# Kernel optimization log

Measured on AMD Instinct MI355X. Metric: run time of the kernel, lower is better.

Reference implementation:

```python
import jax, jax.numpy as jnp
import numpy as np

N = 50000      # nodes in batched graph
E = 800000     # edges
IN_DIM = 16
HID = 64
NH = 4         # heads
G = 128        # graphs in batch
OUT_DIM = 32
NUM_LAYERS = 8
NEG_SLOPE = 0.2  # DGL GATv2Conv default


def setup_inputs() -> dict:
    key = jax.random.key(0)
    ks = jax.random.split(key, 12)
    feat = jax.random.normal(ks[0], (N, IN_DIM), dtype=jnp.float32)
    src = jax.random.randint(ks[1], (E,), 0, N, dtype=jnp.int32)
    dst = jax.random.randint(ks[2], (E,), 0, N, dtype=jnp.int32)
    graph_ids = jnp.sort(jax.random.randint(ks[3], (N,), 0, G, dtype=jnp.int32))
    is_root = jax.random.randint(ks[4], (N,), 0, 2, dtype=jnp.int32)
    s_in = 1.0 / np.sqrt(IN_DIM)
    s_h = 1.0 / np.sqrt(2 * HID)
    s_o = 1.0 / np.sqrt(HID)
    return {
        'feat': feat, 'src': src, 'dst': dst,
        'graph_ids': graph_ids, 'is_root': is_root,
        'W_in': jax.random.normal(ks[5], (IN_DIM, HID), jnp.float32) * s_in,
        'b_in': jnp.zeros((HID,), jnp.float32),
        'W_src': jax.random.normal(ks[6], (2 * HID, NH * HID), jnp.float32) * s_h,
        'b_src': jnp.zeros((NH * HID,), jnp.float32),
        'W_dst': jax.random.normal(ks[7], (2 * HID, NH * HID), jnp.float32) * s_h,
        'b_dst': jnp.zeros((NH * HID,), jnp.float32),
        'attn': jax.random.normal(ks[8], (NH, HID), jnp.float32) * s_o,
        'W_out': jax.random.normal(ks[9], (HID, OUT_DIM), jnp.float32) * s_o,
        'b_out': jnp.zeros((OUT_DIM,), jnp.float32),
    }


def reference(feat, src, dst, graph_ids, is_root,
              W_in, b_in, W_src, b_src, W_dst, b_dst, attn, W_out, b_out):
    h0 = feat @ W_in + b_in                       # [N, HID]
    h = h0
    for _ in range(NUM_LAYERS):
        x = jnp.concatenate([h, h0], axis=1)      # [N, 2*HID]
        fs = (x @ W_src + b_src).reshape(-1, NH, HID)  # [N, NH, HID]
        fd = (x @ W_dst + b_dst).reshape(-1, NH, HID)
        # per-edge GATv2 attention logits
        e = jax.nn.leaky_relu(fs[src] + fd[dst], NEG_SLOPE)   # [E, NH, HID]
        s = jnp.einsum('ehd,hd->eh', e, attn)                 # [E, NH]
        # segment softmax over incoming edges of each dst node
        m = jax.ops.segment_max(s, dst, num_segments=N)       # [N, NH]
        a = jnp.exp(s - m[dst])
        denom = jax.ops.segment_sum(a, dst, num_segments=N)
        alpha = a / denom[dst]                                # [E, NH]
        # weighted aggregation of source features
        agg = jax.ops.segment_sum(alpha[:, :, None] * fs[src], dst,
                                  num_segments=N)             # [N, NH, HID]
        h = jnp.tanh(agg).sum(axis=1)                         # [N, HID]
    # root-weighted readout per graph
    hg = jax.ops.segment_sum(h * is_root.astype(h.dtype)[:, None],
                             graph_ids, num_segments=G)       # [G, HID]
    return hg @ W_out + b_out                                 # [G, OUT_DIM]
```

## Files before the change

kernel.cpp:

```cpp
#include <hip/hip_runtime.h>
#include <math.h>

#define N_NODES 50000
#define N_EDGES 800000
#define IN_DIM  16
#define HID     64
#define NH      4
#define NGRAPH  128
#define OUT_DIM 32
#define NUM_LAYERS 8
#define NEG_SLOPE 0.2f

#define SCAN_BLOCKS ((N_NODES + 255) / 256)

typedef unsigned short u16;
typedef _Float16 h2   __attribute__((ext_vector_type(2)));
typedef _Float16 f16x8 __attribute__((ext_vector_type(8)));
typedef __attribute__((ext_vector_type(4))) float f32x4;

static __device__ __forceinline__ u16 f2h(float f) {
    _Float16 h = (_Float16)f; u16 r; __builtin_memcpy(&r, &h, 2); return r;
}
static __device__ __forceinline__ float h2f_lo(unsigned w) {
    _Float16 h; u16 u = (u16)w; __builtin_memcpy(&h, &u, 2); return (float)h;
}
static __device__ __forceinline__ h2 shfl_h2(h2 v, int mask) {
    int i; __builtin_memcpy(&i, &v, 4); i = __shfl_xor(i, mask);
    h2 r; __builtin_memcpy(&r, &i, 4); return r;
}
static __device__ __forceinline__ h2 bcast_h2(float f) {
    _Float16 h = (_Float16)f; h2 r; r[0] = h; r[1] = h; return r;
}

#define DPP_XOR1(x) __uint_as_float((unsigned)__builtin_amdgcn_update_dpp(0, (int)__float_as_uint(x), 0xB1, 0xF, 0xF, true))
#define DPP_XOR2(x) __uint_as_float((unsigned)__builtin_amdgcn_update_dpp(0, (int)__float_as_uint(x), 0x4E, 0xF, 0xF, true))


__global__ void k_build_wpack(const float* __restrict__ Wsrc, const float* __restrict__ bsrc,
                              const float* __restrict__ Wdst, const float* __restrict__ bdst,
                              const float* __restrict__ attn,
                              u16* __restrict__ Wpack, float* __restrict__ bcat,
                              u16* __restrict__ an_h) {
    int tid = blockIdx.x * 256 + threadIdx.x;
    int i = tid & 7;
    int l = (tid >> 3) & 63;
    int rest = tid >> 9;
    int kt = rest & 3;
    int nt = rest >> 2;
    int k = kt * 32 + (l >> 4) * 8 + i;
    int col = nt * 16 + (l & 15);
    float v = (col < 256) ? Wsrc[k * 256 + col] : Wdst[k * 256 + (col - 256)];
    Wpack[tid] = f2h(v);
    if (tid < 512) bcat[tid] = (tid < 256) ? bsrc[tid] : bdst[tid - 256];
    if (tid < 256) an_h[tid] = f2h(attn[tid] * 1.44269504f);
}

__global__ void k_hist(const int* __restrict__ dst, int* __restrict__ deg) {
    int e = blockIdx.x * 256 + threadIdx.x;
    if (e < N_EDGES) atomicAdd(&deg[dst[e]], 1);
}

__global__ void k_blocksum(const int* __restrict__ deg, int* __restrict__ bsum) {
    __shared__ int sm[256];
    int i = blockIdx.x * 256 + threadIdx.x;
    sm[threadIdx.x] = (i < N_NODES) ? deg[i] : 0;
    __syncthreads();
    for (int s = 128; s > 0; s >>= 1) {
        if (threadIdx.x < s) sm[threadIdx.x] += sm[threadIdx.x + s];
        __syncthreads();
    }
    if (threadIdx.x == 0) bsum[blockIdx.x] = sm[0];
}

__global__ void k_scanbsum(int* __restrict__ bsum) {
    if (threadIdx.x == 0 && blockIdx.x == 0) {
        int acc = 0;
        for (int b = 0; b < SCAN_BLOCKS; b++) { int t = bsum[b]; bsum[b] = acc; acc += t; }
    }
}

__global__ void k_rowptr(const int* __restrict__ deg, const int* __restrict__ bsum,
                         int* __restrict__ row_ptr) {
    __shared__ int sm[256];
    int i = blockIdx.x * 256 + threadIdx.x;
    int v = (i < N_NODES) ? deg[i] : 0;
    sm[threadIdx.x] = v;
    __syncthreads();
    for (int s = 1; s < 256; s <<= 1) {
        int t = (threadIdx.x >= (unsigned)s) ? sm[threadIdx.x - s] : 0;
        __syncthreads();
        sm[threadIdx.x] += t;
        __syncthreads();
    }
    if (i < N_NODES) row_ptr[i] = bsum[blockIdx.x] + sm[threadIdx.x] - v;
}

__global__ void k_scatter(const int* __restrict__ src, const int* __restrict__ dst,
                          const int* __restrict__ row_ptr, int* __restrict__ cursor,
                          int* __restrict__ csr_src) {
    int e = blockIdx.x * 256 + threadIdx.x;
    if (e < N_EDGES) {
        int d = dst[e];
        int pos = atomicAdd(&cursor[d], 1);
        csr_src[row_ptr[d] + pos] = src[e];
    }
}

__global__ __launch_bounds__(256) void k_in_gemm(const float* __restrict__ feat,
                                                 const float* __restrict__ W,
                                                 const float* __restrict__ b,
                                                 u16* __restrict__ h0h) {
    __shared__ float sW[IN_DIM * HID];
    __shared__ float sb[HID];
    int t = threadIdx.x;
    for (int i = t; i < IN_DIM * HID; i += 256) sW[i] = W[i];
    if (t < HID) sb[t] = b[t];
    __syncthreads();
    int wid = (blockIdx.x * 256 + t) >> 6;
    int lane = t & 63;
    const float* f = feat + wid * IN_DIM;
    float acc = sb[lane];
    #pragma unroll
    for (int k = 0; k < IN_DIM; k++) acc += f[k] * sW[k * HID + lane];
    h0h[wid * HID + lane] = f2h(acc);
}


#define ST_STRIDE 152
__global__ __launch_bounds__(256) void k_gemm_mfma(const u16* __restrict__ hb,
                                                   const u16* __restrict__ h0b,
                                                   const u16* __restrict__ Wpack,
                                                   const float* __restrict__ bcat,
                                                   u16* __restrict__ fsfd) {
    __shared__ u16 smem[16384];
    int tid = threadIdx.x;
    int l = tid & 63, w = tid >> 6;
    int lr = l & 15, lg = l >> 4;
    int wave_gid = blockIdx.x * 4 + w;
    size_t rbase = (size_t)wave_gid * 32;
    u16* myst = smem + w * 4096;

    for (int g = 0; g < 4; g++) {
        __syncthreads();
        {
            const f16x8* src = (const f16x8*)(Wpack) + g * 2048;
            f16x8* dst = (f16x8*)smem;
            #pragma unroll
            for (int it = 0; it < 8; it++) dst[it * 256 + tid] = src[it * 256 + tid];
        }
        __syncthreads();

        f32x4 acc[2][8];
        #pragma unroll
        for (int rt = 0; rt < 2; rt++)
            #pragma unroll
            for (int nt = 0; nt < 8; nt++) acc[rt][nt] = (f32x4){0.f, 0.f, 0.f, 0.f};

        #pragma unroll
        for (int kt = 0; kt < 4; kt++) {
            const u16* A = (kt < 2) ? hb : h0b;
            int koff = (kt & 1) * 32 + lg * 8;
            f16x8 a0, a1;
            {
                size_t r0 = rbase + lr;
                size_t r1 = rbase + 16 + lr;
                if (r0 >= N_NODES) r0 = 0;
                if (r1 >= N_NODES) r1 = 0;
                a0 = *(const f16x8*)(A + r0 * HID + koff);
                a1 = *(const f16x8*)(A + r1 * HID + koff);
            }
            #pragma unroll
            for (int nt = 0; nt < 8; nt++) {
                f16x8 bfr = *(const f16x8*)(smem + nt * 2048 + kt * 512 + l * 8);
                acc[0][nt] = __builtin_amdgcn_mfma_f32_16x16x32_f16(a0, bfr, acc[0][nt], 0, 0, 0);
                acc[1][nt] = __builtin_amdgcn_mfma_f32_16x16x32_f16(a1, bfr, acc[1][nt], 0, 0, 0);
            }
        }
        __syncthreads();

        #pragma unroll
        for (int rt = 0; rt < 2; rt++) {
            size_t row0 = rbase + rt * 16;
            if (row0 >= N_NODES) break;
            #pragma unroll
            for (int nt = 0; nt < 8; nt++) {
                float bv = bcat[g * 128 + nt * 16 + lr];
                #pragma unroll
                for (int j = 0; j < 4; j++)
                    myst[(lg * 4 + j) * ST_STRIDE + nt * 16 + lr] = f2h(acc[rt][nt][j] + bv);
            }
            #pragma unroll
            for (int j = 0; j < 4; j++) {
                int rloc = j * 4 + lg;
                f16x8 v = *(const f16x8*)(myst + rloc * ST_STRIDE + lr * 8);
                *(f16x8*)(fsfd + (row0 + rloc) * 512 + g * 128 + lr * 8) = v;
            }
        }
    }
}

__global__ __launch_bounds__(256) void k_edge(const u16* __restrict__ fsfd,
                                              const u16* __restrict__ an_h,
                                              const int* __restrict__ row_ptr,
                                              const int* __restrict__ deg,
                                              const int* __restrict__ csr_src,
                                              u16* __restrict__ h) {
    int wid = (blockIdx.x * 256 + threadIdx.x) >> 6;
    int lane = threadIdx.x & 63;
    int g  = lane >> 4;
    int ll = lane & 15;
    const size_t ebase = (size_t)ll * 16;

    h2 an[8], fdh[8];
    {
        const uint4* ap = (const uint4*)(an_h + ebase);
        uint4 a0 = ap[0], a1 = ap[1];
        unsigned aw[8] = {a0.x, a0.y, a0.z, a0.w, a1.x, a1.y, a1.z, a1.w};
        __builtin_memcpy(an, aw, 32);
        const uint4* fp = (const uint4*)(fsfd + (size_t)wid * 512 + 256 + ebase);
        uint4 b0 = fp[0], b1 = fp[1];
        unsigned fw[8] = {b0.x, b0.y, b0.z, b0.w, b1.x, b1.y, b1.z, b1.w};
        __builtin_memcpy(fdh, fw, 32);
    }
    const h2 slope2 = {(_Float16)NEG_SLOPE, (_Float16)NEG_SLOPE};

    float m = -3.0e38f, denom = 0.f;
    h2 agg[8];
    #pragma unroll
    for (int q = 0; q < 8; q++) agg[q] = (h2){(_Float16)0.f, (_Float16)0.f};

    int r0 = row_ptr[wid], dg = deg[wid];
    for (int i = g; i < dg; i += 4) {
        int s = csr_src[r0 + i];
        const uint4* P = (const uint4*)(fsfd + (size_t)s * 512 + ebase);
        uint4 A = P[0], B = P[1];
        h2 f[8];
        {
            unsigned fw[8] = {A.x, A.y, A.z, A.w, B.x, B.y, B.z, B.w};
            __builtin_memcpy(f, fw, 32);
        }
        float p = 0.f;
        #pragma unroll
        for (int q = 0; q < 8; q++) {
            h2 e  = f[q] + fdh[q];
            h2 lk = __builtin_elementwise_max(e, e * slope2);
#if __has_builtin(__builtin_amdgcn_fdot2)
            p = __builtin_amdgcn_fdot2(lk, an[q], p, false);
#else
            h2 pr = lk * an[q];
            p += (float)pr[0] + (float)pr[1];
#endif
        }
        p += DPP_XOR1(p);
        p += DPP_XOR2(p);
        float nm = fmaxf(m, p);
        float rs = exp2f(m - nm);
        float c  = exp2f(p - nm);
        h2 rs2 = bcast_h2(rs), c2 = bcast_h2(c);
        #pragma unroll
        for (int q = 0; q < 8; q++) agg[q] = agg[q] * rs2 + f[q] * c2;
        denom = fmaf(denom, rs, c);
        m = nm;
    }

    #pragma unroll
    for (int mask = 16; mask <= 32; mask <<= 1) {
        float mo = __shfl_xor(m, mask);
        float dn = __shfl_xor(denom, mask);
        float nm = fmaxf(m, mo);
        float sa = exp2f(m - nm);
        float sb = exp2f(mo - nm);
        h2 sa2 = bcast_h2(sa), sb2 = bcast_h2(sb);
        denom = denom * sa + dn * sb;
        #pragma unroll
        for (int q = 0; q < 8; q++)
            agg[q] = agg[q] * sa2 + shfl_h2(agg[q], mask) * sb2;
        m = nm;
    }

    float inv = denom > 0.f ? __builtin_amdgcn_rcpf(denom) : 0.f;
    float t[16];
    #pragma unroll
    for (int q = 0; q < 8; q++) {
        #pragma unroll
        for (int j = 0; j < 2; j++) {
            float x = (float)agg[q][j] * inv;
            float E = exp2f(x * 2.885390082f);
            float r = __builtin_amdgcn_rcpf(E + 1.f);
            float v = fmaf(-2.f, r, 1.f);
            v += __shfl_xor(v, 4);
            v += __shfl_xor(v, 8);
            t[q * 2 + j] = v;
        }
    }
    if (lane < 4) {
        unsigned o[8];
        #pragma unroll
        for (int q = 0; q < 8; q++)
            o[q] = (unsigned)f2h(t[2*q]) | ((unsigned)f2h(t[2*q+1]) << 16);
        u16* hp = h + (size_t)wid * 64 + lane * 16;
        *(uint4*)hp       = make_uint4(o[0], o[1], o[2], o[3]);
        *(uint4*)(hp + 8) = make_uint4(o[4], o[5], o[6], o[7]);
    }
}


__global__ __launch_bounds__(256) void k_readout(const u16* __restrict__ h,
                                                 const int* __restrict__ graph_ids,
                                                 const int* __restrict__ is_root,
                                                 float* __restrict__ hg) {
    int wid = (blockIdx.x * 256 + threadIdx.x) >> 6;
    int lane = threadIdx.x & 63;
    if (is_root[wid]) {
        int g = graph_ids[wid];
        atomicAdd(&hg[g * HID + lane], h2f_lo(h[(size_t)wid * HID + lane]));
    }
}

__global__ void k_out_gemm(const float* __restrict__ hg, const float* __restrict__ W,
                           const float* __restrict__ b, float* __restrict__ out) {
    int i = blockIdx.x * 256 + threadIdx.x;
    if (i >= NGRAPH * OUT_DIM) return;
    int g = i >> 5, o = i & 31;
    float acc = b[o];
    #pragma unroll
    for (int k = 0; k < HID; k++) acc += hg[g * HID + k] * W[k * OUT_DIM + o];
    out[i] = acc;
}


extern "C" void kernel_launch(void* const* d_in, const int* in_sizes, int n_in,
                              void* d_out, int out_size, void* d_ws, size_t ws_size,
                              hipStream_t stream) {
    const float* feat      = (const float*)d_in[0];
    const int*   src       = (const int*)d_in[1];
    const int*   dst       = (const int*)d_in[2];
    const int*   graph_ids = (const int*)d_in[3];
    const int*   is_root   = (const int*)d_in[4];
    const float* W_in      = (const float*)d_in[5];
    const float* b_in      = (const float*)d_in[6];
    const float* W_src     = (const float*)d_in[7];
    const float* b_src     = (const float*)d_in[8];
    const float* W_dst     = (const float*)d_in[9];
    const float* b_dst     = (const float*)d_in[10];
    const float* attn      = (const float*)d_in[11];
    const float* W_out     = (const float*)d_in[12];
    const float* b_out     = (const float*)d_in[13];
    float* out = (float*)d_out;

    char* base = (char*)d_ws;
    size_t off = 0;
    auto carve = [&](size_t bytes) -> char* {
        char* p = base + off;
        off = (off + bytes + 255) & ~(size_t)255;
        return p;
    };
    u16*   h0b     = (u16*)carve((size_t)N_NODES * HID * 2);
    u16*   hb      = (u16*)carve((size_t)N_NODES * HID * 2);
    u16*   fsfd    = (u16*)carve((size_t)N_NODES * 512 * 2);
    u16*   Wpack   = (u16*)carve(128 * 512 * 2);
    float* bcat    = (float*)carve(512 * 4);
    u16*   an_h    = (u16*)carve(256 * 2);
    int*   csr_src = (int*)carve((size_t)N_EDGES * 4);
    int*   row_ptr = (int*)carve((size_t)N_NODES * 4);
    int*   bsum    = (int*)carve(SCAN_BLOCKS * 4);
    char*  zero0   = carve(0);
    int*   deg     = (int*)carve((size_t)N_NODES * 4);
    int*   cursor  = (int*)carve((size_t)N_NODES * 4);
    float* hg      = (float*)carve((size_t)NGRAPH * HID * 4);
    char*  zero1   = base + off;
    if (off > ws_size) return;

    hipMemsetAsync(zero0, 0, (size_t)(zero1 - zero0), stream);

    k_build_wpack<<<256, 256, 0, stream>>>(W_src, b_src, W_dst, b_dst, attn, Wpack, bcat, an_h);
    k_hist<<<(N_EDGES + 255) / 256, 256, 0, stream>>>(dst, deg);
    k_blocksum<<<SCAN_BLOCKS, 256, 0, stream>>>(deg, bsum);
    k_scanbsum<<<1, 64, 0, stream>>>(bsum);
    k_rowptr<<<SCAN_BLOCKS, 256, 0, stream>>>(deg, bsum, row_ptr);
    k_scatter<<<(N_EDGES + 255) / 256, 256, 0, stream>>>(src, dst, row_ptr, cursor, csr_src);

    k_in_gemm<<<N_NODES / 4, 256, 0, stream>>>(feat, W_in, b_in, h0b);

    const int gemm_grid = (N_NODES + 127) / 128;
    for (int layer = 0; layer < NUM_LAYERS; layer++) {
        const u16* hcur = (layer == 0) ? h0b : hb;
        k_gemm_mfma<<<gemm_grid, 256, 0, stream>>>(hcur, h0b, Wpack, bcat, fsfd);
        k_edge<<<N_NODES / 4, 256, 0, stream>>>(fsfd, an_h, row_ptr, deg, csr_src, hb);
    }

    k_readout<<<N_NODES / 4, 256, 0, stream>>>(hb, graph_ids, is_root, hg);
    k_out_gemm<<<(NGRAPH * OUT_DIM + 255) / 256, 256, 0, stream>>>(hg, W_out, b_out, out);
}
```

Measured before the change: 948.7 us.

## Unroll edge loop two-way with dual softmax accumulators and split tanh epilogue

The per-node attention/aggregation kernel now processes two edges per lane group per iteration, issuing both gathers up front and keeping two independent online-softmax states that are merged after the loop. This gives more memory-level parallelism and shorter dependency chains. The cross-group merge now does a max-rescale followed by plain sums, and the tanh epilogue is split so each lane group computes 4 of the 16 values instead of all 16, cutting redundant transcendental work and shuffles. The cost is higher register pressure and a duplicated, clamped load when the second edge is out of range.

```diff
diff --git a/kernel.cpp b/kernel.cpp
--- a/kernel.cpp
+++ b/kernel.cpp
@@ -224,83 +224,130 @@
     }
     const h2 slope2 = {(_Float16)NEG_SLOPE, (_Float16)NEG_SLOPE};
 
-    float m = -3.0e38f, denom = 0.f;
-    h2 agg[8];
+    float mA = -3.0e38f, mB = -3.0e38f, dnA = 0.f, dnB = 0.f;
+    h2 aggA[8], aggB[8];
     #pragma unroll
-    for (int q = 0; q < 8; q++) agg[q] = (h2){(_Float16)0.f, (_Float16)0.f};
+    for (int q = 0; q < 8; q++) {
+        aggA[q] = (h2){(_Float16)0.f, (_Float16)0.f};
+        aggB[q] = (h2){(_Float16)0.f, (_Float16)0.f};
+    }
 
     int r0 = row_ptr[wid], dg = deg[wid];
-    for (int i = g; i < dg; i += 4) {
-        int s = csr_src[r0 + i];
-        const uint4* P = (const uint4*)(fsfd + (size_t)s * 512 + ebase);
-        uint4 A = P[0], B = P[1];
-        h2 f[8];
+    for (int i = g; i < dg; i += 8) {
+        int iB = i + 4;
+        bool hB = iB < dg;
+        int sA = csr_src[r0 + i];
+        int sB = csr_src[r0 + (hB ? iB : i)];
+        const uint4* PA = (const uint4*)(fsfd + (size_t)sA * 512 + ebase);
+        const uint4* PB = (const uint4*)(fsfd + (size_t)sB * 512 + ebase);
+        uint4 A0 = PA[0], A1 = PA[1];
+        uint4 B0 = PB[0], B1 = PB[1];
+
+        h2 fA[8];
         {
-            unsigned fw[8] = {A.x, A.y, A.z, A.w, B.x, B.y, B.z, B.w};
-            __builtin_memcpy(f, fw, 32);
-        }
-        float p = 0.f;
-        #pragma unroll
-        for (int q = 0; q < 8; q++) {
-            h2 e  = f[q] + fdh[q];
-            h2 lk = __builtin_elementwise_max(e, e * slope2);
-#if __has_builtin(__builtin_amdgcn_fdot2)
-            p = __builtin_amdgcn_fdot2(lk, an[q], p, false);
-#else
-            h2 pr = lk * an[q];
-            p += (float)pr[0] + (float)pr[1];
-#endif
-        }
+            unsigned fw[8] = {A0.x, A0.y, A0.z, A0.w, A1.x, A1.y, A1.z, A1.w};
+            __builtin_memcpy(fA, fw, 32);
+        }
+        float p0 = 0.f, p1 = 0.f;
+        #pragma unroll
+        for (int q = 0; q < 8; q += 2) {
+            h2 e0 = fA[q] + fdh[q];
+            h2 e1 = fA[q+1] + fdh[q+1];
+            h2 l0 = __builtin_elementwise_max(e0, e0 * slope2);
+            h2 l1 = __builtin_elementwise_max(e1, e1 * slope2);
+            p0 = __builtin_amdgcn_fdot2(l0, an[q],   p0, false);
+            p1 = __builtin_amdgcn_fdot2(l1, an[q+1], p1, false);
+        }
+        float p = p0 + p1;
         p += DPP_XOR1(p);
         p += DPP_XOR2(p);
-        float nm = fmaxf(m, p);
-        float rs = exp2f(m - nm);
+        float nm = fmaxf(mA, p);
+        float rs = exp2f(mA - nm);
         float c  = exp2f(p - nm);
         h2 rs2 = bcast_h2(rs), c2 = bcast_h2(c);
         #pragma unroll
-        for (int q = 0; q < 8; q++) agg[q] = agg[q] * rs2 + f[q] * c2;
-        denom = fmaf(denom, rs, c);
-        m = nm;
-    }
-
+        for (int q = 0; q < 8; q++) aggA[q] = aggA[q] * rs2 + fA[q] * c2;
+        dnA = fmaf(dnA, rs, c);
+        mA = nm;
+
+        if (hB) {
+            h2 fB[8];
+            {
+                unsigned fw[8] = {B0.x, B0.y, B0.z, B0.w, B1.x, B1.y, B1.z, B1.w};
+                __builtin_memcpy(fB, fw, 32);
+            }
+            float q0 = 0.f, q1 = 0.f;
+            #pragma unroll
+            for (int q = 0; q < 8; q += 2) {
+                h2 e0 = fB[q] + fdh[q];
+                h2 e1 = fB[q+1] + fdh[q+1];
+                h2 l0 = __builtin_elementwise_max(e0, e0 * slope2);
+                h2 l1 = __builtin_elementwise_max(e1, e1 * slope2);
+                q0 = __builtin_amdgcn_fdot2(l0, an[q],   q0, false);
+                q1 = __builtin_amdgcn_fdot2(l1, an[q+1], q1, false);
+            }
+            float pB = q0 + q1;
+            pB += DPP_XOR1(pB);
+            pB += DPP_XOR2(pB);
+            float nmB = fmaxf(mB, pB);
+            float rsB = exp2f(mB - nmB);
+            float cB  = exp2f(pB - nmB);
+            h2 rsB2 = bcast_h2(rsB), cB2 = bcast_h2(cB);
+            #pragma unroll
+            for (int q = 0; q < 8; q++) aggB[q] = aggB[q] * rsB2 + fB[q] * cB2;
+            dnB = fmaf(dnB, rsB, cB);
+            mB = nmB;
+        }
+    }
+
+    float m, denom;
+    h2 agg[8];
+    {
+        m = fmaxf(mA, mB);
+        float sA = exp2f(mA - m), sB = exp2f(mB - m);
+        denom = dnA * sA + dnB * sB;
+        h2 sA2 = bcast_h2(sA), sB2 = bcast_h2(sB);
+        #pragma unroll
+        for (int q = 0; q < 8; q++) agg[q] = aggA[q] * sA2 + aggB[q] * sB2;
+    }
+
+    {
+        float mm = fmaxf(m, __shfl_xor(m, 16));
+        mm = fmaxf(mm, __shfl_xor(mm, 32));
+        float sc = exp2f(m - mm);
+        denom *= sc;
+        h2 sc2 = bcast_h2(sc);
+        #pragma unroll
+        for (int q = 0; q < 8; q++) agg[q] = agg[q] * sc2;
+        denom += __shfl_xor(denom, 16);
+        denom += __shfl_xor(denom, 32);
+        #pragma unroll
+        for (int q = 0; q < 8; q++) {
+            agg[q] = agg[q] + shfl_h2(agg[q], 16);
+            agg[q] = agg[q] + shfl_h2(agg[q], 32);
+        }
+    }
+
+    float inv = denom > 0.f ? __builtin_amdgcn_rcpf(denom) : 0.f;
+    float inv2 = inv * 2.885390082f;
+
+    h2 x0 = (g & 2) ? ((g & 1) ? agg[6] : agg[4]) : ((g & 1) ? agg[2] : agg[0]);
+    h2 x1 = (g & 2) ? ((g & 1) ? agg[7] : agg[5]) : ((g & 1) ? agg[3] : agg[1]);
+    float t[4] = {(float)x0[0], (float)x0[1], (float)x1[0], (float)x1[1]};
     #pragma unroll
-    for (int mask = 16; mask <= 32; mask <<= 1) {
-        float mo = __shfl_xor(m, mask);
-        float dn = __shfl_xor(denom, mask);
-        float nm = fmaxf(m, mo);
-        float sa = exp2f(m - nm);
-        float sb = exp2f(mo - nm);
-        h2 sa2 = bcast_h2(sa), sb2 = bcast_h2(sb);
-        denom = denom * sa + dn * sb;
-        #pragma unroll
-        for (int q = 0; q < 8; q++)
-            agg[q] = agg[q] * sa2 + shfl_h2(agg[q], mask) * sb2;
-        m = nm;
-    }
-
-    float inv = denom > 0.f ? __builtin_amdgcn_rcpf(denom) : 0.f;
-    float t[16];
-    #pragma unroll
-    for (int q = 0; q < 8; q++) {
-        #pragma unroll
-        for (int j = 0; j < 2; j++) {
-            float x = (float)agg[q][j] * inv;
-            float E = exp2f(x * 2.885390082f);
-            float r = __builtin_amdgcn_rcpf(E + 1.f);
-            float v = fmaf(-2.f, r, 1.f);
-            v += __shfl_xor(v, 4);
-            v += __shfl_xor(v, 8);
-            t[q * 2 + j] = v;
-        }
-    }
-    if (lane < 4) {
-        unsigned o[8];
-        #pragma unroll
-        for (int q = 0; q < 8; q++)
-            o[q] = (unsigned)f2h(t[2*q]) | ((unsigned)f2h(t[2*q+1]) << 16);
-        u16* hp = h + (size_t)wid * 64 + lane * 16;
-        *(uint4*)hp       = make_uint4(o[0], o[1], o[2], o[3]);
-        *(uint4*)(hp + 8) = make_uint4(o[4], o[5], o[6], o[7]);
+    for (int j = 0; j < 4; j++) {
+        float E = exp2f(t[j] * inv2);
+        float r = __builtin_amdgcn_rcpf(E + 1.f);
+        float v = fmaf(-2.f, r, 1.f);
+        v += __shfl_xor(v, 4);
+        v += __shfl_xor(v, 8);
+        t[j] = v;
+    }
+    if (ll < 4) {
+        uint2 o;
+        o.x = (unsigned)f2h(t[0]) | ((unsigned)f2h(t[1]) << 16);
+        o.y = (unsigned)f2h(t[2]) | ((unsigned)f2h(t[3]) << 16);
+        *(uint2*)(h + (size_t)wid * 64 + ll * 16 + g * 4) = o;
     }
 }
 
```

Result: slower. 989.9 us (+4.3%).
